# Kernel tuning notes

Measured on AMD Instinct MI355X. Metric: run time of the kernel, lower is better.

The kernel has to match this reference:

```python
import jax, jax.numpy as jnp
import numpy as np

SEQ = 180 - 1  # hardcoded in original forward

def setup_inputs() -> dict:
    key = jax.random.key(0)
    k1, k2, k3 = jax.random.split(key, 3)
    B, V = 32, 9487
    N = B * SEQ
    seqLogprobs = jax.random.normal(k1, (B, SEQ, V), dtype=jnp.float32)
    reward = jax.random.uniform(k2, (N,), dtype=jnp.float32)
    target = jax.random.randint(k3, (N,), 0, V, dtype=jnp.int64)
    return {"seqLogprobs": seqLogprobs, "reward": reward,
            "batchsize_cap": 32, "target": target}

def reference(seqLogprobs, reward, batchsize_cap, target):
    # Flatten to (N, V) exactly like .view(batchsize_cap*(180-1), -1)
    N = batchsize_cap * SEQ
    logp = seqLogprobs.reshape(N, -1)
    # one_hot scatter + masked_select is just a per-row gather by target index
    picked = jnp.take_along_axis(logp, target.reshape(N, 1), axis=1)[:, 0]
    loss = -jnp.sum(picked * reward.reshape(-1))
    return loss
```

## Files before the change

kernel.cpp:

```cpp
#include <hip/hip_runtime.h>
#include <hip/hip_bf16.h>

__global__ __launch_bounds__(1024) void
RewardCriterion2_kernel(const float* __restrict__ logp,
                        const float* __restrict__ reward,
                        const int* __restrict__ target,
                        float* __restrict__ out,
                        int N, int V) {
    float acc = 0.0f;
    for (int i = threadIdx.x; i < N; i += 1024) {
        long long idx = (long long)i * (long long)V + (long long)target[i];
        acc += logp[idx] * reward[i];
    }

    #pragma unroll
    for (int off = 32; off > 0; off >>= 1) {
        acc += __shfl_down(acc, off, 64);
    }

    __shared__ float warp_sums[16];
    const int lane = threadIdx.x & 63;
    const int wave = threadIdx.x >> 6;
    if (lane == 0) warp_sums[wave] = acc;
    __syncthreads();

    if (threadIdx.x == 0) {
        float total = 0.0f;
        #pragma unroll
        for (int w = 0; w < 16; ++w) total += warp_sums[w];
        out[0] = -total;
    }
}

extern "C" void kernel_launch(void* const* d_in, const int* in_sizes, int n_in,
                              void* d_out, int out_size, void* d_ws, size_t ws_size,
                              hipStream_t stream) {
    const float* logp   = (const float*)d_in[0];
    const float* reward = (const float*)d_in[1];
    const int*   target = (const int*)d_in[3];

    float* out = (float*)d_out;

    const int N = in_sizes[1];
    const int V = in_sizes[0] / N;

    RewardCriterion2_kernel<<<1, 1024, 0, stream>>>(logp, reward, target, out, N, V);
}
```

Baseline: 258.1 us.

## Split gather-reduce across many blocks with a two-pass reduction

Replaces the single 1024-thread block with one thread per row across many 256-thread blocks. Each block writes a partial sum to workspace, and a small second kernel reduces the partials. The goal is to expose more memory-level parallelism across CUs for the scattered gathers, instead of serialising them on one CU. It adds a second kernel launch, and the finalize step assumes at most 64 partial blocks.

```diff
diff --git a/kernel.cpp b/kernel.cpp
--- a/kernel.cpp
+++ b/kernel.cpp
@@ -1,35 +1,44 @@
 #include <hip/hip_runtime.h>
 #include <hip/hip_bf16.h>
 
-__global__ __launch_bounds__(1024) void
-RewardCriterion2_kernel(const float* __restrict__ logp,
-                        const float* __restrict__ reward,
-                        const int* __restrict__ target,
-                        float* __restrict__ out,
-                        int N, int V) {
-    float acc = 0.0f;
-    for (int i = threadIdx.x; i < N; i += 1024) {
-        long long idx = (long long)i * (long long)V + (long long)target[i];
-        acc += logp[idx] * reward[i];
+
+__global__ __launch_bounds__(256) void
+gather_partial(const float* __restrict__ logp,
+               const float* __restrict__ reward,
+               const int* __restrict__ target,
+               float* __restrict__ partial,
+               int N, int V) {
+    const int i = blockIdx.x * 256 + threadIdx.x;
+    float v = 0.0f;
+    if (i < N) {
+        const long long idx = (long long)i * (long long)V + (long long)target[i];
+        v = logp[idx] * reward[i];
     }
 
     #pragma unroll
     for (int off = 32; off > 0; off >>= 1) {
-        acc += __shfl_down(acc, off, 64);
+        v += __shfl_down(v, off, 64);
     }
 
-    __shared__ float warp_sums[16];
+    __shared__ float wsum[4];
     const int lane = threadIdx.x & 63;
     const int wave = threadIdx.x >> 6;
-    if (lane == 0) warp_sums[wave] = acc;
+    if (lane == 0) wsum[wave] = v;
     __syncthreads();
 
     if (threadIdx.x == 0) {
-        float total = 0.0f;
-        #pragma unroll
-        for (int w = 0; w < 16; ++w) total += warp_sums[w];
-        out[0] = -total;
+        partial[blockIdx.x] = wsum[0] + wsum[1] + wsum[2] + wsum[3];
     }
+}
+
+__global__ __launch_bounds__(64) void
+finalize(const float* __restrict__ partial, float* __restrict__ out, int nb) {
+    float v = (threadIdx.x < (unsigned)nb) ? partial[threadIdx.x] : 0.0f;
+    #pragma unroll
+    for (int off = 32; off > 0; off >>= 1) {
+        v += __shfl_down(v, off, 64);
+    }
+    if (threadIdx.x == 0) out[0] = -v;
 }
 
 extern "C" void kernel_launch(void* const* d_in, const int* in_sizes, int n_in,
@@ -40,9 +49,12 @@
     const int*   target = (const int*)d_in[3];
 
     float* out = (float*)d_out;
+    float* partial = (float*)d_ws;
 
     const int N = in_sizes[1];
     const int V = in_sizes[0] / N;
+    const int nb = (N + 255) / 256;
 
-    RewardCriterion2_kernel<<<1, 1024, 0, stream>>>(logp, reward, target, out, N, V);
+    gather_partial<<<nb, 256, 0, stream>>>(logp, reward, target, partial, N, V);
+    finalize<<<1, 64, 0, stream>>>(partial, out, nb);
 }
```

Measured after the change: 246.4 us. 1.05x faster.
